# Kernel tuning notes

Measured on AMD Instinct MI355X. Metric: run time of the kernel, lower is better.

## Reference

```python
import jax, jax.numpy as jnp
import numpy as np

N, E = 50000, 800000
D_IN, D_HID, D_OUT = 128, 128, 64


def sage_conv(x, src, dst, w_l, w_r, b, n_nodes):
    # PyG SAGEConv (aggr='mean', root_weight=True):
    #   out = lin_l(mean_{j in N(i)} x_j) + lin_r(x_i)
    msg_sum = jax.ops.segment_sum(x[src], dst, num_segments=n_nodes)  # [N, d]
    cnt = jax.ops.segment_sum(jnp.ones((src.shape[0],), x.dtype), dst,
                              num_segments=n_nodes)                   # [N]
    mean = msg_sum / jnp.maximum(cnt, 1.0)[:, None]
    return mean @ w_l.T + x @ w_r.T + b


def prelu(x, a):
    return jnp.maximum(x, 0) + a * jnp.minimum(x, 0)


def setup_inputs() -> dict:
    key = jax.random.key(0)
    ks = jax.random.split(key, 12)
    def lin(k, o, i):
        s = 1.0 / np.sqrt(i)
        return jax.random.uniform(k, (o, i), jnp.float32, -s, s)
    x = jax.random.normal(ks[0], (N, D_IN), jnp.float32)
    edge_index = jax.random.randint(ks[1], (2, E), 0, N, jnp.int64)
    return {
        "x": x,
        "edge_index": edge_index,
        "w1l": lin(ks[2], D_HID, D_IN),  "w1r": lin(ks[3], D_HID, D_IN),
        "b1": jnp.zeros((D_HID,), jnp.float32),
        "w2l": lin(ks[4], D_HID, D_HID), "w2r": lin(ks[5], D_HID, D_HID),
        "b2": jnp.zeros((D_HID,), jnp.float32),
        "w3l": lin(ks[6], D_OUT, D_HID), "w3r": lin(ks[7], D_OUT, D_HID),
        "b3": jnp.zeros((D_OUT,), jnp.float32),
        "a": jnp.array(0.25, jnp.float32),  # shared PReLU slope
        "wp": lin(ks[8], 1, D_OUT),
        "bp": jnp.zeros((1,), jnp.float32),
    }


def reference(x, edge_index, w1l, w1r, b1, w2l, w2r, b2, w3l, w3r, b3, a, wp, bp):
    src, dst = edge_index[0], edge_index[1]
    n = x.shape[0]
    h = prelu(sage_conv(x, src, dst, w1l, w1r, b1, n), a)
    h = prelu(sage_conv(h, src, dst, w2l, w2r, b2, n), a)
    h = sage_conv(h, src, dst, w3l, w3r, b3, n)          # [N, D_OUT]
    level = (h @ wp.T + bp).squeeze(-1)                  # [N]
    return level
```

## Files before the change

### kernel.cpp

```cpp
#include <hip/hip_runtime.h>
#include <cstdint>
#include <cstddef>

typedef float f32x4 __attribute__((ext_vector_type(4)));
typedef short short8 __attribute__((ext_vector_type(8)));
typedef __bf16 bf16x8 __attribute__((ext_vector_type(8)));

__device__ __forceinline__ void mfma_bf16(f32x4& d, short8 a, short8 b){
  d = __builtin_amdgcn_mfma_f32_16x16x32_bf16(
        __builtin_bit_cast(bf16x8, a), __builtin_bit_cast(bf16x8, b), d, 0, 0, 0);
}

__device__ __forceinline__ unsigned short bf16_rn(float f){
  unsigned u = __float_as_uint(f);
  unsigned r = (u + 0x7FFF + ((u >> 16) & 1)) >> 16;
  return (unsigned short)r;
}

__device__ __forceinline__ int blockScan256Excl(int v, int* wsum){
  const int lane = threadIdx.x & 63, wv = threadIdx.x >> 6;
  int x = v;
  #pragma unroll
  for (int off = 1; off < 64; off <<= 1){
    int y = __shfl_up(x, off);
    if (lane >= off) x += y;
  }
  if (lane == 63) wsum[wv] = x;
  __syncthreads();
  int woff = 0;
  #pragma unroll
  for (int w = 0; w < 4; ++w) woff += (w < wv) ? wsum[w] : 0;
  return woff + x - v;
}

__global__ __launch_bounds__(256) void k_bcount(const int* __restrict__ dst, int E, int nb, int ntiles,
                                                int* __restrict__ blk_hist){
  __shared__ int h[256];
  const int tile = blockIdx.x;
  h[threadIdx.x] = 0;
  __syncthreads();
  const int base = tile * 2048;
  const int end = min(base + 2048, E);
  for (int i = base + threadIdx.x; i < end; i += 256)
    atomicAdd(&h[dst[i] >> 8], 1);
  __syncthreads();
  const int b = threadIdx.x;
  if (b < nb) blk_hist[(size_t)b * ntiles + tile] = h[b];
}

__global__ __launch_bounds__(256) void k_bscan(int* __restrict__ blk_hist, int nb, int ntiles,
                                               int* __restrict__ tot){
  __shared__ int wsum[4];
  __shared__ int carry;
  const int b = blockIdx.x;
  int* row = blk_hist + (size_t)b * ntiles;
  if (threadIdx.x == 0) carry = 0;
  __syncthreads();
  const int lane = threadIdx.x & 63, wv = threadIdx.x >> 6;
  for (int base = 0; base < ntiles; base += 256){
    const int i = base + threadIdx.x;
    const int v = (i < ntiles) ? row[i] : 0;
    int x = v;
    #pragma unroll
    for (int off = 1; off < 64; off <<= 1){
      int y = __shfl_up(x, off);
      if (lane >= off) x += y;
    }
    if (lane == 63) wsum[wv] = x;
    __syncthreads();
    int woff = 0;
    #pragma unroll
    for (int w = 0; w < 4; ++w) woff += (w < wv) ? wsum[w] : 0;
    const int incl = carry + woff + x;
    if (i < ntiles) row[i] = incl - v;
    __syncthreads();
    if (threadIdx.x == 255) carry = incl;
    __syncthreads();
  }
  if (threadIdx.x == 0) tot[b] = carry;
}

__global__ __launch_bounds__(256) void k_btot(const int* __restrict__ tot, int nb,
                                              int* __restrict__ bucket_base){
  __shared__ int wsum[4];
  const int t = threadIdx.x;
  const int v = (t < nb) ? tot[t] : 0;
  const int e = blockScan256Excl(v, wsum);
  if (t <= nb) bucket_base[t] = e;
}

__global__ __launch_bounds__(256) void k_bscat(const int* __restrict__ src, const int* __restrict__ dst,
                                               int E, int nb, int ntiles,
                                               const int* __restrict__ blk_off,
                                               const int* __restrict__ bucket_base,
                                               unsigned* __restrict__ ebuf){
  __shared__ int cnt[256];
  __shared__ int lofs[256];
  __shared__ int gbase[256];
  __shared__ unsigned sorted[2048];
  __shared__ unsigned char sb[2048];
  __shared__ int wsum[4];
  const int tile = blockIdx.x;
  cnt[threadIdx.x] = 0;
  __syncthreads();
  const int base = tile * 2048;
  const int end = min(base + 2048, E);
  const int m = end - base;

  int rank_[8]; int b_[8]; unsigned v_[8];
  #pragma unroll
  for (int k = 0; k < 8; ++k){
    const int j = threadIdx.x + k * 256;
    if (base + j < end){
      const int d = dst[base + j];
      const int s = src[base + j];
      const int b = d >> 8;
      b_[k] = b;
      v_[k] = ((unsigned)(d & 255) << 16) | (unsigned)s;
      rank_[k] = atomicAdd(&cnt[b], 1);
    } else b_[k] = -1;
  }
  __syncthreads();
  const int ex = blockScan256Excl(cnt[threadIdx.x], wsum);
  lofs[threadIdx.x] = ex;
  if (threadIdx.x < nb)
    gbase[threadIdx.x] = bucket_base[threadIdx.x] + blk_off[(size_t)threadIdx.x * ntiles + tile];
  __syncthreads();
  #pragma unroll
  for (int k = 0; k < 8; ++k){
    if (b_[k] >= 0){
      const int p = lofs[b_[k]] + rank_[k];
      sorted[p] = v_[k];
      sb[p] = (unsigned char)b_[k];
    }
  }
  __syncthreads();
  for (int j = threadIdx.x; j < m; j += 256){
    const int b = sb[j];
    ebuf[gbase[b] + (j - lofs[b])] = sorted[j];
  }
}

__global__ __launch_bounds__(256) void k_csrfin(const unsigned* __restrict__ ebuf,
                                                const int* __restrict__ bucket_base,
                                                int n, int E, int nb,
                                                int* __restrict__ row_ptr,
                                                float* __restrict__ inv,
                                                unsigned short* __restrict__ csr){
  __shared__ int hist[256], excl[256], cursor[256];
  __shared__ int wsum[4];
  __shared__ unsigned vals[8192];
  __shared__ unsigned short sorted[8192];
  const int b = blockIdx.x;
  const int ebase = bucket_base[b];
  const int ecnt = bucket_base[b + 1] - ebase;
  const int t = threadIdx.x;
  hist[t] = 0;
  __syncthreads();
  for (int j = t; j < ecnt; j += 256){
    const unsigned v = ebuf[ebase + j];
    vals[j] = v;
    atomicAdd(&hist[v >> 16], 1);
  }
  __syncthreads();
  const int ex = blockScan256Excl(hist[t], wsum);
  excl[t] = ex;
  cursor[t] = ex;
  const int node = b * 256 + t;
  if (node < n){
    row_ptr[node] = ebase + ex;
    const int c = hist[t];
    inv[node] = 1.0f / (float)(c > 0 ? c : 1);
  }
  if (b == nb - 1 && t == 0) row_ptr[n] = E;
  __syncthreads();
  for (int j = t; j < ecnt; j += 256){
    const unsigned v = vals[j];
    const int pos = atomicAdd(&cursor[v >> 16], 1);
    sorted[pos] = (unsigned short)(v & 0xFFFFu);
  }
  __syncthreads();
  for (int j = t; j < ecnt; j += 256)
    csr[ebase + j] = sorted[j];
}

__global__ __launch_bounds__(256) void k_cvt(const float* __restrict__ in,
                                             unsigned short* __restrict__ out, int total){
  const int i = (blockIdx.x * 256 + threadIdx.x) * 4;
  if (i >= total) return;
  const float4 v = *(const float4*)&in[i];
  ushort2 a, b;
  a.x = bf16_rn(v.x); a.y = bf16_rn(v.y);
  b.x = bf16_rn(v.z); b.y = bf16_rn(v.w);
  *(ushort2*)&out[i] = a;
  *(ushort2*)&out[i + 2] = b;
}

__global__ __launch_bounds__(256) void k_aggb(const unsigned short* __restrict__ featb,
                                              const unsigned short* __restrict__ csr,
                                              const int* __restrict__ row_ptr,
                                              const float* __restrict__ inv_cnt,
                                              float* __restrict__ outb, int n){
  const int lane = threadIdx.x & 63;
  const int node = (blockIdx.x * blockDim.x + threadIdx.x) >> 6;
  if (node >= n) return;
  const int beg = row_ptr[node];
  const int end = row_ptr[node + 1];
  const unsigned* __restrict__ fb = (const unsigned*)featb;

  float ax0=0.f, ay0=0.f, ax1=0.f, ay1=0.f, ax2=0.f, ay2=0.f, ax3=0.f, ay3=0.f;
  float ax4=0.f, ay4=0.f, ax5=0.f, ay5=0.f, ax6=0.f, ay6=0.f, ax7=0.f, ay7=0.f;

  int j = beg;
  for (; j + 8 <= end; j += 8){
    const int s0 = csr[j+0], s1 = csr[j+1], s2 = csr[j+2], s3 = csr[j+3];
    const int s4 = csr[j+4], s5 = csr[j+5], s6 = csr[j+6], s7 = csr[j+7];
    const unsigned u0 = fb[(size_t)s0 * 64 + lane];
    const unsigned u1 = fb[(size_t)s1 * 64 + lane];
    const unsigned u2 = fb[(size_t)s2 * 64 + lane];
    const unsigned u3 = fb[(size_t)s3 * 64 + lane];
    const unsigned u4 = fb[(size_t)s4 * 64 + lane];
    const unsigned u5 = fb[(size_t)s5 * 64 + lane];
    const unsigned u6 = fb[(size_t)s6 * 64 + lane];
    const unsigned u7 = fb[(size_t)s7 * 64 + lane];
    ax0 += __uint_as_float(u0 << 16); ay0 += __uint_as_float(u0 & 0xFFFF0000u);
    ax1 += __uint_as_float(u1 << 16); ay1 += __uint_as_float(u1 & 0xFFFF0000u);
    ax2 += __uint_as_float(u2 << 16); ay2 += __uint_as_float(u2 & 0xFFFF0000u);
    ax3 += __uint_as_float(u3 << 16); ay3 += __uint_as_float(u3 & 0xFFFF0000u);
    ax4 += __uint_as_float(u4 << 16); ay4 += __uint_as_float(u4 & 0xFFFF0000u);
    ax5 += __uint_as_float(u5 << 16); ay5 += __uint_as_float(u5 & 0xFFFF0000u);
    ax6 += __uint_as_float(u6 << 16); ay6 += __uint_as_float(u6 & 0xFFFF0000u);
    ax7 += __uint_as_float(u7 << 16); ay7 += __uint_as_float(u7 & 0xFFFF0000u);
  }
  if (j + 4 <= end){
    const int s0 = csr[j+0], s1 = csr[j+1], s2 = csr[j+2], s3 = csr[j+3];
    const unsigned u0 = fb[(size_t)s0 * 64 + lane];
    const unsigned u1 = fb[(size_t)s1 * 64 + lane];
    const unsigned u2 = fb[(size_t)s2 * 64 + lane];
    const unsigned u3 = fb[(size_t)s3 * 64 + lane];
    ax0 += __uint_as_float(u0 << 16); ay0 += __uint_as_float(u0 & 0xFFFF0000u);
    ax1 += __uint_as_float(u1 << 16); ay1 += __uint_as_float(u1 & 0xFFFF0000u);
    ax2 += __uint_as_float(u2 << 16); ay2 += __uint_as_float(u2 & 0xFFFF0000u);
    ax3 += __uint_as_float(u3 << 16); ay3 += __uint_as_float(u3 & 0xFFFF0000u);
    j += 4;
  }
  for (; j < end; ++j){
    const int s = csr[j];
    const unsigned u = fb[(size_t)s * 64 + lane];
    ax4 += __uint_as_float(u << 16); ay4 += __uint_as_float(u & 0xFFFF0000u);
  }

  const float ic = inv_cnt[node];
  float2 o;
  o.x = (((ax0 + ax1) + (ax2 + ax3)) + ((ax4 + ax5) + (ax6 + ax7))) * ic;
  o.y = (((ay0 + ay1) + (ay2 + ay3)) + ((ay4 + ay5) + (ay6 + ay7))) * ic;
  *(float2*)&outb[(size_t)node * 128 + lane * 2] = o;
}

__global__ void k_wcs(const float* __restrict__ wl, const float* __restrict__ wr,
                      short* __restrict__ bfr){
  int id = blockIdx.x * 256 + threadIdx.x;
  if (id >= 128 * 256) return;
  int c = id >> 8, k = id & 255;
  float w = (k < 128) ? wl[c * 128 + k] : wr[c * 128 + (k - 128)];
  unsigned short h = bf16_rn(w);
  float hf = __uint_as_float((unsigned)h << 16);
  unsigned short l = bf16_rn(w - hf);
  const int nt = c >> 4, mrow = c & 15;
  const int ks = k >> 5, kgrp = (k >> 3) & 3, j = k & 7;
  const int lane = kgrp * 16 + mrow;
  const size_t fbase = (size_t)((ks * 8 + nt) * 2) * 512 + lane * 8 + j;
  bfr[fbase] = (short)h;
  bfr[fbase + 512] = (short)l;
}

__global__ __launch_bounds__(256) void k_gemm_mfma(const float* __restrict__ A0,
                                                   const float* __restrict__ A1,
                                                   const short* __restrict__ bfr,
                                                   const float* __restrict__ bias,
                                                   const float* __restrict__ alpha_p,
                                                   float* __restrict__ out,
                                                   unsigned short* __restrict__ outb16,
                                                   int n){
  const int t = threadIdx.x;
  const int lane = t & 63;
  const int wv = t >> 6;
  const int nodeBase = blockIdx.x * 64 + wv * 16;
  const int mrow = lane & 15;
  const int kgrp = lane >> 4;

  int node = nodeBase + mrow;
  if (node > n - 1) node = n - 1;
  const size_t arow = (size_t)node * 128;

  const short8* __restrict__ Bf = (const short8*)bfr;

  f32x4 acc[8];
  #pragma unroll
  for (int i = 0; i < 8; ++i) acc[i] = (f32x4){0.f, 0.f, 0.f, 0.f};

  #pragma unroll
  for (int ks = 0; ks < 8; ++ks){
    const float* __restrict__ Asrc = (ks < 4) ? A0 : A1;
    const int kk = (ks & 3) * 32 + kgrp * 8;
    const float4 v0 = *(const float4*)&Asrc[arow + kk];
    const float4 v1 = *(const float4*)&Asrc[arow + kk + 4];

    short8 bh[8], bl[8];
    const int fb = ks * 16;
    #pragma unroll
    for (int nt = 0; nt < 8; ++nt){
      bh[nt] = Bf[(size_t)(fb + nt * 2 + 0) * 64 + lane];
      bl[nt] = Bf[(size_t)(fb + nt * 2 + 1) * 64 + lane];
    }

    const float av[8] = {v0.x, v0.y, v0.z, v0.w, v1.x, v1.y, v1.z, v1.w};
    short8 ah, al;
    #pragma unroll
    for (int i = 0; i < 8; ++i){
      unsigned short h = bf16_rn(av[i]);
      ah[i] = (short)h;
      float hf = __uint_as_float((unsigned)h << 16);
      al[i] = (short)bf16_rn(av[i] - hf);
    }

    #pragma unroll
    for (int nt = 0; nt < 8; ++nt){
      mfma_bf16(acc[nt], ah, bh[nt]);
      mfma_bf16(acc[nt], al, bh[nt]);
      mfma_bf16(acc[nt], ah, bl[nt]);
    }
  }

  const float alpha = *alpha_p;
  #pragma unroll
  for (int nt = 0; nt < 8; ++nt){
    const int col = nt * 16 + mrow;
    const float bv = bias[col];
    #pragma unroll
    for (int j = 0; j < 4; ++j){
      const int onode = nodeBase + kgrp * 4 + j;
      if (onode < n){
        float v = acc[nt][j] + bv;
        v = fmaxf(v, 0.f) + alpha * fminf(v, 0.f);
        out[(size_t)onode * 128 + col] = v;
        if (outb16) outb16[(size_t)onode * 128 + col] = bf16_rn(v);
      }
    }
  }
}

__global__ void k_u(const float* __restrict__ w3l, const float* __restrict__ w3r,
                    const float* __restrict__ b3, const float* __restrict__ wp,
                    const float* __restrict__ bp, float* __restrict__ u){
  int k = threadIdx.x;
  float sl = 0.f, sr = 0.f;
  for (int o = 0; o < 64; ++o){
    float w = wp[o];
    sl = fmaf(w, w3l[o * 128 + k], sl);
    sr = fmaf(w, w3r[o * 128 + k], sr);
  }
  u[k] = sl; u[128 + k] = sr;
  if (k == 0){
    float c = bp[0];
    for (int o = 0; o < 64; ++o) c = fmaf(wp[o], b3[o], c);
    u[256] = c;
  }
}

__global__ __launch_bounds__(256) void k_dot(const float* __restrict__ h,
                                             const float* __restrict__ u,
                                             float* __restrict__ s,
                                             float* __restrict__ partial, int n){
  const int lane = threadIdx.x & 63;
  const int i = blockIdx.x * 4 + (threadIdx.x >> 6);
  if (i >= n) return;
  const float2 hv  = *(const float2*)&h[(size_t)i * 128 + lane * 2];
  const float2 ulv = *(const float2*)&u[lane * 2];
  const float2 urv = *(const float2*)&u[128 + lane * 2];
  float sv = hv.x * ulv.x + hv.y * ulv.y;
  float tv = hv.x * urv.x + hv.y * urv.y;
  #pragma unroll
  for (int off = 32; off > 0; off >>= 1){
    sv += __shfl_down(sv, off);
    tv += __shfl_down(tv, off);
  }
  if (lane == 0){ s[i] = sv; partial[i] = tv + u[256]; }
}

__global__ __launch_bounds__(256) void k_final(const float* __restrict__ s, const float* __restrict__ partial,
                        const unsigned short* __restrict__ csr, const int* __restrict__ row_ptr,
                        const float* __restrict__ inv_cnt, float* __restrict__ out, int n){
  const int t = blockIdx.x * blockDim.x + threadIdx.x;
  const int node = t >> 2;
  const int sub = t & 3;
  if (node >= n) return;
  const int b = row_ptr[node], e = row_ptr[node + 1];
  float a0 = 0.f, a1 = 0.f;
  int j = b + sub;
  for (; j + 4 < e; j += 8){
    a0 += s[csr[j]];
    a1 += s[csr[j + 4]];
  }
  if (j < e) a0 += s[csr[j]];
  float acc = a0 + a1;
  acc += __shfl_down(acc, 1);
  acc += __shfl_down(acc, 2);
  if (sub == 0) out[node] = acc * inv_cnt[node] + partial[node];
}

extern "C" void kernel_launch(void* const* d_in, const int* in_sizes, int n_in,
                              void* d_out, int out_size, void* d_ws, size_t ws_size,
                              hipStream_t stream){
  const float* x   = (const float*)d_in[0];
  const int*   ei  = (const int*)d_in[1];
  const float* w1l = (const float*)d_in[2];
  const float* w1r = (const float*)d_in[3];
  const float* b1  = (const float*)d_in[4];
  const float* w2l = (const float*)d_in[5];
  const float* w2r = (const float*)d_in[6];
  const float* b2  = (const float*)d_in[7];
  const float* w3l = (const float*)d_in[8];
  const float* w3r = (const float*)d_in[9];
  const float* b3  = (const float*)d_in[10];
  const float* ap  = (const float*)d_in[11];
  const float* wp  = (const float*)d_in[12];
  const float* bp  = (const float*)d_in[13];

  const int n = out_size;
  const int E = in_sizes[1] / 2;
  const int* srcI = ei;
  const int* dstI = ei + E;

  const int ntiles = (E + 2047) / 2048;
  const int nb = (n + 255) >> 8;

  char* base = (char*)d_ws;
  size_t off = 0;
  auto take = [&](size_t bytes) -> char* {
    off = (off + 255) & ~(size_t)255;
    char* p = base + off;
    off += bytes;
    return p;
  };
  int*      blk_hist = (int*)   take((size_t)nb * ntiles * 4);
  int*      tot      = (int*)   take((size_t)nb * 4);
  int*      bbase    = (int*)   take(((size_t)nb + 1) * 4);
  unsigned* ebuf     = (unsigned*)take((size_t)E * 4);
  int*      rowp     = (int*)   take(((size_t)n + 1) * 4);
  float*    inv      = (float*) take((size_t)n * 4);
  unsigned short* csr = (unsigned short*)take((size_t)E * 2);
  float*    B1   = (float*)take((size_t)n * 128 * 4);
  float*    B2   = (float*)take((size_t)n * 128 * 4);
  unsigned short* xb  = (unsigned short*)take((size_t)n * 128 * 2);
  unsigned short* h1b = (unsigned short*)take((size_t)n * 128 * 2);
  float*    sbuf = (float*)take((size_t)n * 4);
  float*    pbuf = (float*)take((size_t)n * 4);
  float*    u    = (float*)take(257 * 4);
  short*    bfr  = (short*)take((size_t)128 * 512 * 2);
  (void)ws_size; (void)n_in;

  k_bcount<<<ntiles, 256, 0, stream>>>(dstI, E, nb, ntiles, blk_hist);
  k_bscan <<<nb,     256, 0, stream>>>(blk_hist, nb, ntiles, tot);
  k_btot  <<<1,      256, 0, stream>>>(tot, nb, bbase);
  k_bscat <<<ntiles, 256, 0, stream>>>(srcI, dstI, E, nb, ntiles, blk_hist, bbase, ebuf);
  k_csrfin<<<nb,     256, 0, stream>>>(ebuf, bbase, n, E, nb, rowp, inv, csr);

  k_cvt<<<(n * 128 / 4 + 255) / 256, 256, 0, stream>>>(x, xb, n * 128);

  const int aggGrid  = (n * 64 + 255) / 256;
  const int gemmGrid = (n + 63) / 64;

  k_aggb     <<<aggGrid, 256, 0, stream>>>(xb, csr, rowp, inv, B1, n);
  k_wcs      <<<128, 256, 0, stream>>>(w1l, w1r, bfr);
  k_gemm_mfma<<<gemmGrid, 256, 0, stream>>>(B1, x, bfr, b1, ap, B2, h1b, n);

  k_aggb     <<<aggGrid, 256, 0, stream>>>(h1b, csr, rowp, inv, B1, n);
  k_wcs      <<<128, 256, 0, stream>>>(w2l, w2r, bfr);
  k_gemm_mfma<<<gemmGrid, 256, 0, stream>>>(B1, B2, bfr, b2, ap, B2, (unsigned short*)nullptr, n);

  k_u    <<<1, 128, 0, stream>>>(w3l, w3r, b3, wp, bp, u);
  k_dot  <<<(n + 3) / 4, 256, 0, stream>>>(B2, u, sbuf, pbuf, n);
  k_final<<<(n * 4 + 255) / 256, 256, 0, stream>>>(sbuf, pbuf, csr, rowp, inv, (float*)d_out, n);
}
```

Measured before the change: 190.5 us.

## Store aggregates in bf16 and stage bf16 GEMM A-tiles through swizzled LDS

The aggregation kernel now writes bf16 instead of fp32, and both GEMMs read bf16 A operands (aggregate plus bf16 copies of x and h1). Each block stages them into XOR-swizzled shared memory instead of loading fp32 rows and splitting them into hi/lo bf16 per lane. The A-side split is dropped, so each tile needs two MFMAs instead of three, and layer one no longer writes an fp32 copy of its output. This cuts global traffic and MFMA work, at the cost of lower precision on activations and extra LDS use per block.

```diff
diff --git a/kernel.cpp b/kernel.cpp
--- a/kernel.cpp
+++ b/kernel.cpp
@@ -200,7 +200,7 @@
                                               const unsigned short* __restrict__ csr,
                                               const int* __restrict__ row_ptr,
                                               const float* __restrict__ inv_cnt,
-                                              float* __restrict__ outb, int n){
+                                              unsigned short* __restrict__ outb, int n){
   const int lane = threadIdx.x & 63;
   const int node = (blockIdx.x * blockDim.x + threadIdx.x) >> 6;
   if (node >= n) return;
@@ -251,10 +251,10 @@
   }
 
   const float ic = inv_cnt[node];
-  float2 o;
-  o.x = (((ax0 + ax1) + (ax2 + ax3)) + ((ax4 + ax5) + (ax6 + ax7))) * ic;
-  o.y = (((ay0 + ay1) + (ay2 + ay3)) + ((ay4 + ay5) + (ay6 + ay7))) * ic;
-  *(float2*)&outb[(size_t)node * 128 + lane * 2] = o;
+  const float ox = (((ax0 + ax1) + (ax2 + ax3)) + ((ax4 + ax5) + (ax6 + ax7))) * ic;
+  const float oy = (((ay0 + ay1) + (ay2 + ay3)) + ((ay4 + ay5) + (ay6 + ay7))) * ic;
+  const unsigned packed = (unsigned)bf16_rn(ox) | ((unsigned)bf16_rn(oy) << 16);
+  ((unsigned*)outb)[(size_t)node * 64 + lane] = packed;
 }
 
 __global__ void k_wcs(const float* __restrict__ wl, const float* __restrict__ wr,
@@ -274,26 +274,40 @@
   bfr[fbase + 512] = (short)l;
 }
 
-__global__ __launch_bounds__(256) void k_gemm_mfma(const float* __restrict__ A0,
-                                                   const float* __restrict__ A1,
+__global__ __launch_bounds__(256) void k_gemm_mfma(const unsigned short* __restrict__ A0b,
+                                                   const unsigned short* __restrict__ A1b,
                                                    const short* __restrict__ bfr,
                                                    const float* __restrict__ bias,
                                                    const float* __restrict__ alpha_p,
-                                                   float* __restrict__ out,
+                                                   float* __restrict__ outf,
                                                    unsigned short* __restrict__ outb16,
                                                    int n){
+  __shared__ short aT[2][64 * 128];
   const int t = threadIdx.x;
   const int lane = t & 63;
   const int wv = t >> 6;
-  const int nodeBase = blockIdx.x * 64 + wv * 16;
+  const int nodeBase = blockIdx.x * 64;
+
+  #pragma unroll
+  for (int tab = 0; tab < 2; ++tab){
+    const unsigned short* __restrict__ src = tab ? A1b : A0b;
+    #pragma unroll
+    for (int it = 0; it < 4; ++it){
+      const int chunk = it * 256 + t;
+      const int row = chunk >> 4;
+      const int slot = chunk & 15;
+      int gr = nodeBase + row; if (gr > n - 1) gr = n - 1;
+      const uint4 v = *(const uint4*)&src[(size_t)gr * 128 + slot * 8];
+      const int sslot = slot ^ (row & 7);
+      *(uint4*)((char*)&aT[tab][0] + row * 256 + sslot * 16) = v;
+    }
+  }
+  __syncthreads();
+
+  const short8* __restrict__ Bf = (const short8*)bfr;
   const int mrow = lane & 15;
   const int kgrp = lane >> 4;
-
-  int node = nodeBase + mrow;
-  if (node > n - 1) node = n - 1;
-  const size_t arow = (size_t)node * 128;
-
-  const short8* __restrict__ Bf = (const short8*)bfr;
+  const int arow = wv * 16 + mrow;
 
   f32x4 acc[8];
   #pragma unroll
@@ -301,10 +315,9 @@
 
   #pragma unroll
   for (int ks = 0; ks < 8; ++ks){
-    const float* __restrict__ Asrc = (ks < 4) ? A0 : A1;
-    const int kk = (ks & 3) * 32 + kgrp * 8;
-    const float4 v0 = *(const float4*)&Asrc[arow + kk];
-    const float4 v1 = *(const float4*)&Asrc[arow + kk + 4];
+    const int tab = ks >> 2;
+    const int slot_r = (ks & 3) * 4 + kgrp;
+    const short8 aF = *(const short8*)((const char*)&aT[tab][0] + arow * 256 + (slot_r ^ (arow & 7)) * 16);
 
     short8 bh[8], bl[8];
     const int fb = ks * 16;
@@ -313,37 +326,26 @@
       bh[nt] = Bf[(size_t)(fb + nt * 2 + 0) * 64 + lane];
       bl[nt] = Bf[(size_t)(fb + nt * 2 + 1) * 64 + lane];
     }
-
-    const float av[8] = {v0.x, v0.y, v0.z, v0.w, v1.x, v1.y, v1.z, v1.w};
-    short8 ah, al;
-    #pragma unroll
-    for (int i = 0; i < 8; ++i){
-      unsigned short h = bf16_rn(av[i]);
-      ah[i] = (short)h;
-      float hf = __uint_as_float((unsigned)h << 16);
-      al[i] = (short)bf16_rn(av[i] - hf);
-    }
-
     #pragma unroll
     for (int nt = 0; nt < 8; ++nt){
-      mfma_bf16(acc[nt], ah, bh[nt]);
-      mfma_bf16(acc[nt], al, bh[nt]);
-      mfma_bf16(acc[nt], ah, bl[nt]);
+      mfma_bf16(acc[nt], aF, bh[nt]);
+      mfma_bf16(acc[nt], aF, bl[nt]);
     }
   }
 
   const float alpha = *alpha_p;
+  const int nodeQ = nodeBase + wv * 16 + kgrp * 4;
   #pragma unroll
   for (int nt = 0; nt < 8; ++nt){
     const int col = nt * 16 + mrow;
     const float bv = bias[col];
     #pragma unroll
     for (int j = 0; j < 4; ++j){
-      const int onode = nodeBase + kgrp * 4 + j;
+      const int onode = nodeQ + j;
       if (onode < n){
         float v = acc[nt][j] + bv;
         v = fmaxf(v, 0.f) + alpha * fminf(v, 0.f);
-        out[(size_t)onode * 128 + col] = v;
+        if (outf)   outf[(size_t)onode * 128 + col] = v;
         if (outb16) outb16[(size_t)onode * 128 + col] = bf16_rn(v);
       }
     }
@@ -450,7 +452,7 @@
   int*      rowp     = (int*)   take(((size_t)n + 1) * 4);
   float*    inv      = (float*) take((size_t)n * 4);
   unsigned short* csr = (unsigned short*)take((size_t)E * 2);
-  float*    B1   = (float*)take((size_t)n * 128 * 4);
+  unsigned short* B1b = (unsigned short*)take((size_t)n * 128 * 2);
   float*    B2   = (float*)take((size_t)n * 128 * 4);
   unsigned short* xb  = (unsigned short*)take((size_t)n * 128 * 2);
   unsigned short* h1b = (unsigned short*)take((size_t)n * 128 * 2);
@@ -471,13 +473,13 @@
   const int aggGrid  = (n * 64 + 255) / 256;
   const int gemmGrid = (n + 63) / 64;
 
-  k_aggb     <<<aggGrid, 256, 0, stream>>>(xb, csr, rowp, inv, B1, n);
+  k_aggb     <<<aggGrid, 256, 0, stream>>>(xb, csr, rowp, inv, B1b, n);
   k_wcs      <<<128, 256, 0, stream>>>(w1l, w1r, bfr);
-  k_gemm_mfma<<<gemmGrid, 256, 0, stream>>>(B1, x, bfr, b1, ap, B2, h1b, n);
-
-  k_aggb     <<<aggGrid, 256, 0, stream>>>(h1b, csr, rowp, inv, B1, n);
+  k_gemm_mfma<<<gemmGrid, 256, 0, stream>>>(B1b, xb, bfr, b1, ap, (float*)nullptr, h1b, n);
+
+  k_aggb     <<<aggGrid, 256, 0, stream>>>(h1b, csr, rowp, inv, B1b, n);
   k_wcs      <<<128, 256, 0, stream>>>(w2l, w2r, bfr);
-  k_gemm_mfma<<<gemmGrid, 256, 0, stream>>>(B1, B2, bfr, b2, ap, B2, (unsigned short*)nullptr, n);
+  k_gemm_mfma<<<gemmGrid, 256, 0, stream>>>(B1b, h1b, bfr, b2, ap, B2, (unsigned short*)nullptr, n);
 
   k_u    <<<1, 128, 0, stream>>>(w3l, w3r, b3, wp, bp, u);
   k_dot  <<<(n + 3) / 4, 256, 0, stream>>>(B2, u, sbuf, pbuf, n);
```

Result: faster. 178.7 us (-6.2%).
